# Performance work log

Hardware: AMD Instinct MI355X
Metric: run time of the kernel (lower is better)

## Reference

```python
import jax, jax.numpy as jnp
import numpy as np

N, E, IN_DIM, H, C = 100000, 1600000, 128, 4, 64
NEG_SLOPE = 0.2
BN_EPS = 1e-5


def setup_inputs() -> dict:
    key = jax.random.key(0)
    ks = jax.random.split(key, 9)
    s = 1.0 / np.sqrt(IN_DIM)
    return {
        "feature": jax.random.normal(ks[0], (N, IN_DIM), dtype=jnp.float32),
        "edge_index": jax.random.randint(ks[1], (2, E), 0, N, dtype=jnp.int64),
        "W_l": jax.random.uniform(ks[2], (IN_DIM, H * C), jnp.float32, -s, s),
        "b_l": jnp.zeros((H * C,), jnp.float32),
        "W_r": jax.random.uniform(ks[3], (IN_DIM, H * C), jnp.float32, -s, s),
        "b_r": jnp.zeros((H * C,), jnp.float32),
        "att": jax.random.normal(ks[4], (H, C), dtype=jnp.float32) * 0.1,
        "bias": jnp.zeros((H * C,), jnp.float32),
        "gamma": jnp.ones((H * C,), jnp.float32),
        "beta": jnp.zeros((H * C,), jnp.float32),
    }


def reference(feature, edge_index, W_l, b_l, W_r, b_r, att, bias, gamma, beta):
    n = feature.shape[0]
    # add self loops (add_self_loops=True)
    loops = jnp.arange(n, dtype=edge_index.dtype)
    src = jnp.concatenate([edge_index[0], loops])
    dst = jnp.concatenate([edge_index[1], loops])
    # GATv2: separate source/target linear projections -> [N, H, C]
    x_l = (feature @ W_l + b_l).reshape(n, H, C)
    x_r = (feature @ W_r + b_r).reshape(n, H, C)
    # per-edge attention score: a^T LeakyReLU(x_l[src] + x_r[dst])  [Etot, H]
    e = jax.nn.leaky_relu(x_l[src] + x_r[dst], NEG_SLOPE)
    alpha = jnp.einsum('ehc,hc->eh', e, att)
    # segment softmax over incoming edges per target node
    amax = jax.ops.segment_max(alpha, dst, num_segments=n)  # [N, H]
    alpha = jnp.exp(alpha - amax[dst])
    denom = jax.ops.segment_sum(alpha, dst, num_segments=n)  # [N, H]
    alpha = alpha / (denom[dst] + 1e-16)
    # weighted scatter-aggregate of source messages
    out = jax.ops.segment_sum(x_l[src] * alpha[:, :, None], dst, num_segments=n)
    out = out.reshape(n, H * C) + bias  # concat=True
    # BatchNorm1d (training: batch statistics over nodes)
    mean = out.mean(axis=0)
    var = out.var(axis=0)
    out = (out - mean) / jnp.sqrt(var + BN_EPS) * gamma + beta
    return jax.nn.relu(out)
```

## Files before the change

### kernel.cpp

```cpp
#include <hip/hip_runtime.h>
#include <cstdint>

#define IN_DIM 128
#define HC 256
#define NEG_SLOPE 0.2f
#define BN_EPS 1e-5f
#define LOG2E 1.44269504088896340736f

#define B_HIST 1536
#define B_CW 32
#define B_FILL 512

typedef short bf16x8 __attribute__((ext_vector_type(8)));
typedef float f32x4 __attribute__((ext_vector_type(4)));

#define EXP2F(x) __builtin_amdgcn_exp2f(x)

__device__ __forceinline__ unsigned short f2bf(float f) {
    union { float f; unsigned int u; } v; v.f = f;
    unsigned int r = (v.u + 0x7FFFu + ((v.u >> 16) & 1u)) >> 16;
    return (unsigned short)r;
}
__device__ __forceinline__ float bf2f(unsigned short h) {
    union { unsigned int u; float f; } v; v.u = ((unsigned int)h) << 16;
    return v.f;
}

template<int CTRL>
__device__ __forceinline__ float dppadd(float x) {
    int y = __builtin_amdgcn_update_dpp(0, __builtin_bit_cast(int, x), CTRL, 0xF, 0xF, true);
    return x + __builtin_bit_cast(float, y);
}
__device__ __forceinline__ float red16(float p) {
    p = dppadd<0xB1>(p);
    p = dppadd<0x4E>(p);
    p = dppadd<0x124>(p);
    p = dppadd<0x128>(p);
    return p;
}

__device__ __forceinline__ void unpk(ushort4 u, float* f) {
    f[0] = bf2f(u.x); f[1] = bf2f(u.y); f[2] = bf2f(u.z); f[3] = bf2f(u.w);
}
__device__ __forceinline__ float esc(const float* f, float x0, float x1, float x2, float x3,
                                     float4 a) {
    float z0 = f[0] + x0, z1 = f[1] + x1, z2 = f[2] + x2, z3 = f[3] + x3;
    float p = a.x * fmaxf(z0, NEG_SLOPE * z0);
    p = fmaf(a.y, fmaxf(z1, NEG_SLOPE * z1), p);
    p = fmaf(a.z, fmaxf(z2, NEG_SLOPE * z2), p);
    p = fmaf(a.w, fmaxf(z3, NEG_SLOPE * z3), p);
    return p;
}

__global__ __launch_bounds__(256) void phase1(
    const float* __restrict__ F, unsigned short* __restrict__ Afrag,
    const float* __restrict__ Wl, const float* __restrict__ Wr,
    unsigned short* __restrict__ Wfrag,
    const int* __restrict__ ei, int* __restrict__ cnt, int* __restrict__ rank,
    int E, int n, int ntiles)
{
    int b = blockIdx.x;
    if (b < B_HIST) {
        int total = E + n;
        for (int e = b * 256 + threadIdx.x; e < total; e += B_HIST * 256) {
            int dst = (e < E) ? ei[(size_t)E + e] : (e - E);
            rank[e] = atomicAdd(&cnt[dst], 1);
        }
    } else if (b < B_HIST + B_CW) {
        int ob = (b - B_HIST) * 4 + (threadIdx.x >> 6);
        int j = ob >> 2;
        int kk = ob & 3;
        int l = threadIdx.x & 63;
        int col = j * 16 + (l & 15);
        const float* W = (col < 256) ? Wl : Wr;
        int c = col & 255;
        unsigned short tmp[8];
#pragma unroll
        for (int m = 0; m < 8; ++m) {
            int k = kk * 32 + ((l >> 4) << 3) + m;
            tmp[m] = f2bf(W[(size_t)k * 256 + c]);
        }
        ulonglong2* dst = (ulonglong2*)(Wfrag + ((size_t)(j * 4 + kk) * 64 + l) * 8);
        *dst = *(ulonglong2*)tmp;
    } else {
        int i = b - B_HIST - B_CW;
        int kk = threadIdx.x >> 6;
        int l = threadIdx.x & 63;
        int row = i * 16 + (l & 15);
        int k0 = kk * 32 + ((l >> 4) << 3);
        float4 f0 = make_float4(0.f, 0.f, 0.f, 0.f), f1 = f0;
        if (row < n) {
            const float* p = F + (size_t)row * IN_DIM + k0;
            f0 = *(const float4*)p;
            f1 = *(const float4*)(p + 4);
        }
        unsigned short tmp[8];
        tmp[0] = f2bf(f0.x); tmp[1] = f2bf(f0.y); tmp[2] = f2bf(f0.z); tmp[3] = f2bf(f0.w);
        tmp[4] = f2bf(f1.x); tmp[5] = f2bf(f1.y); tmp[6] = f2bf(f1.z); tmp[7] = f2bf(f1.w);
        ulonglong2* dst = (ulonglong2*)(Afrag + ((size_t)(i * 4 + kk) * 64 + l) * 8);
        *dst = *(ulonglong2*)tmp;
    }
}

#define SCAN_BLOCKS 256

__global__ __launch_bounds__(256) void scan_phaseA(const int* __restrict__ cnt,
                                                   int* __restrict__ blocksums,
                                                   int n, int ept)
{
    __shared__ int red[256];
    int t = threadIdx.x;
    int g = blockIdx.x * 256 + t;
    int beg = g * ept, end = min(beg + ept, n);
    int s = 0;
    for (int i = beg; i < end; ++i) s += cnt[i];
    red[t] = s;
    __syncthreads();
    for (int d = 128; d > 0; d >>= 1) {
        if (t < d) red[t] += red[t + d];
        __syncthreads();
    }
    if (t == 0) blocksums[blockIdx.x] = red[0];
}

__global__ __launch_bounds__(256) void scan_phaseB(const int* __restrict__ blocksums,
                                                   int* __restrict__ blockoffs,
                                                   int* __restrict__ off, int n)
{
    __shared__ int sums[256];
    int t = threadIdx.x;
    sums[t] = blocksums[t];
    __syncthreads();
    for (int d = 1; d < 256; d <<= 1) {
        int v = (t >= d) ? sums[t - d] : 0;
        __syncthreads();
        sums[t] += v;
        __syncthreads();
    }
    blockoffs[t] = (t == 0) ? 0 : sums[t - 1];
    if (t == 255) off[n] = sums[255];
}

__global__ __launch_bounds__(256) void scan_phaseC(const int* __restrict__ cnt,
                                                   const int* __restrict__ blockoffs,
                                                   int* __restrict__ off,
                                                   int n, int ept)
{
    __shared__ int sums[256];
    int t = threadIdx.x;
    int g = blockIdx.x * 256 + t;
    int beg = g * ept, end = min(beg + ept, n);
    int s = 0;
    for (int i = beg; i < end; ++i) s += cnt[i];
    sums[t] = s;
    __syncthreads();
    for (int d = 1; d < 256; d <<= 1) {
        int v = (t >= d) ? sums[t - d] : 0;
        __syncthreads();
        sums[t] += v;
        __syncthreads();
    }
    int run = blockoffs[blockIdx.x] + ((t == 0) ? 0 : sums[t - 1]);
    for (int i = beg; i < end; ++i) {
        int c = cnt[i];
        off[i] = run;
        run += c;
    }
}

__global__ __launch_bounds__(256) void phase2(
    const unsigned short* __restrict__ Afrag, const unsigned short* __restrict__ Wfrag,
    const float* __restrict__ bl, const float* __restrict__ br,
    unsigned short* __restrict__ xl, unsigned short* __restrict__ xr,
    const int* __restrict__ ei, const int* __restrict__ rank,
    const int* __restrict__ off, int* __restrict__ csr_boff,
    int E, int n, int ntiles)
{
    int b = blockIdx.x;
    if (b < B_FILL) {
        int total = E + n;
        for (int e = b * 256 + threadIdx.x; e < total; e += B_FILL * 256) {
            int src, dst;
            if (e < E) { src = ei[e]; dst = ei[(size_t)E + e]; }
            else       { src = dst = e - E; }
            int pos = off[dst] + rank[e];
            csr_boff[pos] = src << 9;
        }
    } else {
        int i = (b - B_FILL) * 4 + (threadIdx.x >> 6);
        if (i >= ntiles) return;
        int l = threadIdx.x & 63;

        const bf16x8* av = (const bf16x8*)(Afrag + ((size_t)i * 4 * 64 + l) * 8);
        bf16x8 a0 = av[0 * 64], a1 = av[1 * 64], a2 = av[2 * 64], a3 = av[3 * 64];

        const bf16x8* wv = (const bf16x8*)Wfrag + l;
        int cl = l & 15;
        int rbase = i * 16 + ((l >> 4) << 2);

#pragma unroll 4
        for (int j = 0; j < 32; ++j) {
            const bf16x8* bp = wv + (size_t)j * 4 * 64;
            f32x4 acc = {0.f, 0.f, 0.f, 0.f};
            acc = __builtin_amdgcn_mfma_f32_16x16x32_bf16(a0, bp[0 * 64], acc, 0, 0, 0);
            acc = __builtin_amdgcn_mfma_f32_16x16x32_bf16(a1, bp[1 * 64], acc, 0, 0, 0);
            acc = __builtin_amdgcn_mfma_f32_16x16x32_bf16(a2, bp[2 * 64], acc, 0, 0, 0);
            acc = __builtin_amdgcn_mfma_f32_16x16x32_bf16(a3, bp[3 * 64], acc, 0, 0, 0);

            int col = j * 16 + cl;
            unsigned short* X = (col < 256) ? xl : xr;
            int c = col & 255;
            float bv = (col < 256) ? bl[c] : br[c];
#pragma unroll
            for (int q = 0; q < 4; ++q) {
                int row = rbase + q;
                if (row < n) X[(size_t)row * HC + c] = f2bf(acc[q] + bv);
            }
        }
    }
}

__global__ __launch_bounds__(256) void gat_agg(
    const unsigned short* __restrict__ xl, const unsigned short* __restrict__ xr,
    const int* __restrict__ csr_boff, const int* __restrict__ off,
    const float* __restrict__ att, const float* __restrict__ bias,
    float* __restrict__ out, int n)
{
    int d = (blockIdx.x * blockDim.x + threadIdx.x) >> 6;
    int lane = threadIdx.x & 63;
    if (d >= n) return;

    const char* xlc = (const char*)xl;
    int lo8 = lane << 3;
    ushort4 xru = ((const ushort4*)xr)[(size_t)d * 64 + lane];
    float xr0 = bf2f(xru.x), xr1 = bf2f(xru.y), xr2 = bf2f(xru.z), xr3 = bf2f(xru.w);
    float4 att4 = *(const float4*)(att + 4 * lane);
    att4.x *= LOG2E; att4.y *= LOG2E; att4.z *= LOG2E; att4.w *= LOG2E;

    int beg = __builtin_amdgcn_readfirstlane(off[d]);
    int end = __builtin_amdgcn_readfirstlane(off[d + 1]);
    float m = -INFINITY;
    float lsum = 0.f;
    float ax = 0.f, ay = 0.f, az = 0.f, aw = 0.f;

    int i = beg;
    for (; i + 3 < end; i += 4) {
        int b0 = __builtin_amdgcn_readfirstlane(csr_boff[i]);
        int b1 = __builtin_amdgcn_readfirstlane(csr_boff[i + 1]);
        int b2 = __builtin_amdgcn_readfirstlane(csr_boff[i + 2]);
        int b3 = __builtin_amdgcn_readfirstlane(csr_boff[i + 3]);
        ushort4 u0 = *(const ushort4*)(xlc + b0 + lo8);
        ushort4 u1 = *(const ushort4*)(xlc + b1 + lo8);
        ushort4 u2 = *(const ushort4*)(xlc + b2 + lo8);
        ushort4 u3 = *(const ushort4*)(xlc + b3 + lo8);
        float f0[4], f1[4], f2[4], f3[4];
        unpk(u0, f0); unpk(u1, f1); unpk(u2, f2); unpk(u3, f3);

        float p0 = esc(f0, xr0, xr1, xr2, xr3, att4);
        float p1 = esc(f1, xr0, xr1, xr2, xr3, att4);
        float p2 = esc(f2, xr0, xr1, xr2, xr3, att4);
        float p3 = esc(f3, xr0, xr1, xr2, xr3, att4);

        p0 = dppadd<0xB1>(p0);  p1 = dppadd<0xB1>(p1);  p2 = dppadd<0xB1>(p2);  p3 = dppadd<0xB1>(p3);
        p0 = dppadd<0x4E>(p0);  p1 = dppadd<0x4E>(p1);  p2 = dppadd<0x4E>(p2);  p3 = dppadd<0x4E>(p3);
        p0 = dppadd<0x124>(p0); p1 = dppadd<0x124>(p1); p2 = dppadd<0x124>(p2); p3 = dppadd<0x124>(p3);
        p0 = dppadd<0x128>(p0); p1 = dppadd<0x128>(p1); p2 = dppadd<0x128>(p2); p3 = dppadd<0x128>(p3);

        float mx = fmaxf(fmaxf(p0, p1), fmaxf(p2, p3));
        if (mx > m) {
            float sc = EXP2F(m - mx);
            ax *= sc; ay *= sc; az *= sc; aw *= sc; lsum *= sc;
            m = mx;
        }
        float e0 = EXP2F(p0 - m), e1 = EXP2F(p1 - m);
        float e2 = EXP2F(p2 - m), e3 = EXP2F(p3 - m);
        ax = fmaf(e0, f0[0], fmaf(e1, f1[0], fmaf(e2, f2[0], fmaf(e3, f3[0], ax))));
        ay = fmaf(e0, f0[1], fmaf(e1, f1[1], fmaf(e2, f2[1], fmaf(e3, f3[1], ay))));
        az = fmaf(e0, f0[2], fmaf(e1, f1[2], fmaf(e2, f2[2], fmaf(e3, f3[2], az))));
        aw = fmaf(e0, f0[3], fmaf(e1, f1[3], fmaf(e2, f2[3], fmaf(e3, f3[3], aw))));
        lsum += (e0 + e1) + (e2 + e3);
    }
    for (; i < end; ++i) {
        int b0 = __builtin_amdgcn_readfirstlane(csr_boff[i]);
        ushort4 u0 = *(const ushort4*)(xlc + b0 + lo8);
        float f0[4];
        unpk(u0, f0);
        float p0 = esc(f0, xr0, xr1, xr2, xr3, att4);
        p0 = red16(p0);
        if (p0 > m) {
            float sc = EXP2F(m - p0);
            ax *= sc; ay *= sc; az *= sc; aw *= sc; lsum *= sc;
            m = p0;
        }
        float e0 = EXP2F(p0 - m);
        ax = fmaf(e0, f0[0], ax); ay = fmaf(e0, f0[1], ay);
        az = fmaf(e0, f0[2], az); aw = fmaf(e0, f0[3], aw);
        lsum += e0;
    }

    float inv = 1.f / (lsum + 1e-16f);
    float4 b4 = *(const float4*)(bias + 4 * lane);
    float4 o;
    o.x = fmaf(ax, inv, b4.x); o.y = fmaf(ay, inv, b4.y);
    o.z = fmaf(az, inv, b4.z); o.w = fmaf(aw, inv, b4.w);
    *(float4*)(out + (size_t)d * HC + 4 * lane) = o;
}

#define NB_BN 1024
__global__ __launch_bounds__(256) void bn_partial(const float* __restrict__ out,
                                                  float* __restrict__ partials, int n)
{
    int c = threadIdx.x;
    int b = blockIdx.x;
    int chunk = (n + NB_BN - 1) / NB_BN;
    int beg = b * chunk;
    int end = min(beg + chunk, n);
    float s = 0.f, s2 = 0.f;
    for (int r = beg; r < end; ++r) {
        float v = out[(size_t)r * HC + c];
        s += v; s2 += v * v;
    }
    partials[(size_t)b * 512 + c] = s;
    partials[(size_t)b * 512 + 256 + c] = s2;
}

__global__ __launch_bounds__(256) void bn_final(const float* __restrict__ partials,
                                                float* __restrict__ stats, int n)
{
    int c = blockIdx.x;
    int t = threadIdx.x;
    float s = 0.f, s2 = 0.f;
    for (int b = t; b < NB_BN; b += 256) {
        s  += partials[(size_t)b * 512 + c];
        s2 += partials[(size_t)b * 512 + 256 + c];
    }
    __shared__ float rs[256], rs2[256];
    rs[t] = s; rs2[t] = s2;
    __syncthreads();
    for (int d = 128; d > 0; d >>= 1) {
        if (t < d) { rs[t] += rs[t + d]; rs2[t] += rs2[t + d]; }
        __syncthreads();
    }
    if (t == 0) {
        float mean = rs[0] / (float)n;
        float var = rs2[0] / (float)n - mean * mean;
        stats[c] = mean;
        stats[256 + c] = rsqrtf(var + BN_EPS);
    }
}

__global__ void bn_apply(float* __restrict__ out, const float* __restrict__ stats,
                         const float* __restrict__ gamma, const float* __restrict__ beta,
                         long long total4)
{
    long long stride = (long long)gridDim.x * blockDim.x;
    for (long long i = blockIdx.x * (long long)blockDim.x + threadIdx.x; i < total4;
         i += stride) {
        int cb = ((int)(i & 63)) * 4;
        float4 v = ((const float4*)out)[i];
        float4 o;
        o.x = fmaxf(0.f, (v.x - stats[cb + 0]) * stats[256 + cb + 0] * gamma[cb + 0] + beta[cb + 0]);
        o.y = fmaxf(0.f, (v.y - stats[cb + 1]) * stats[256 + cb + 1] * gamma[cb + 1] + beta[cb + 1]);
        o.z = fmaxf(0.f, (v.z - stats[cb + 2]) * stats[256 + cb + 2] * gamma[cb + 2] + beta[cb + 2]);
        o.w = fmaxf(0.f, (v.w - stats[cb + 3]) * stats[256 + cb + 3] * gamma[cb + 3] + beta[cb + 3]);
        ((float4*)out)[i] = o;
    }
}

extern "C" void kernel_launch(void* const* d_in, const int* in_sizes, int n_in,
                              void* d_out, int out_size, void* d_ws, size_t ws_size,
                              hipStream_t stream)
{
    const float* feature = (const float*)d_in[0];
    const int* ei        = (const int*)d_in[1];
    const float* Wl   = (const float*)d_in[2];
    const float* bl   = (const float*)d_in[3];
    const float* Wr   = (const float*)d_in[4];
    const float* br   = (const float*)d_in[5];
    const float* att  = (const float*)d_in[6];
    const float* bias = (const float*)d_in[7];
    const float* gamma = (const float*)d_in[8];
    const float* beta  = (const float*)d_in[9];

    const int n = in_sizes[0] / IN_DIM;
    const int E = in_sizes[1] / 2;
    const int Etot = E + n;
    const int ntiles = (n + 15) / 16;

    char* ws = (char*)d_ws;
    size_t o = 0;
    auto carve = [&](size_t bytes) -> void* {
        void* p = ws + o; o = (o + bytes + 15) & ~(size_t)15; return p;
    };
    unsigned short* xl    = (unsigned short*)carve((size_t)n * HC * sizeof(short));
    unsigned short* xr    = (unsigned short*)carve((size_t)n * HC * sizeof(short));
    unsigned short* Afrag = (unsigned short*)carve((size_t)ntiles * 4 * 64 * 8 * sizeof(short));
    unsigned short* Wfrag = (unsigned short*)carve((size_t)32 * 4 * 64 * 8 * sizeof(short));
    int*   csr_boff = (int*)carve((size_t)Etot * sizeof(int));
    int*   rank    = (int*)carve((size_t)Etot * sizeof(int));
    int*   cnt     = (int*)carve((size_t)n * sizeof(int));
    int*   off     = (int*)carve((size_t)(n + 1) * sizeof(int));
    int*   blocksums = (int*)carve(SCAN_BLOCKS * sizeof(int));
    int*   blockoffs = (int*)carve(SCAN_BLOCKS * sizeof(int));
    float* partials = (float*)carve((size_t)NB_BN * 512 * sizeof(float));
    float* stats   = (float*)carve(512 * sizeof(float));
    float* outf = (float*)d_out;

    if (o > ws_size) return;

    (void)hipMemsetAsync(cnt, 0, (size_t)n * sizeof(int), stream);

    phase1<<<B_HIST + B_CW + ntiles, 256, 0, stream>>>(
        feature, Afrag, Wl, Wr, Wfrag, ei, cnt, rank, E, n, ntiles);

    int ept = (n + SCAN_BLOCKS * 256 - 1) / (SCAN_BLOCKS * 256);
    scan_phaseA<<<SCAN_BLOCKS, 256, 0, stream>>>(cnt, blocksums, n, ept);
    scan_phaseB<<<1, 256, 0, stream>>>(blocksums, blockoffs, off, n);
    scan_phaseC<<<SCAN_BLOCKS, 256, 0, stream>>>(cnt, blockoffs, off, n, ept);

    phase2<<<B_FILL + (ntiles + 3) / 4, 256, 0, stream>>>(
        Afrag, Wfrag, bl, br, xl, xr, ei, rank, off, csr_boff, E, n, ntiles);

    int agg_blocks = (n + 3) / 4;
    gat_agg<<<agg_blocks, 256, 0, stream>>>(xl, xr, csr_boff, off, att, bias, outf, n);

    bn_partial<<<NB_BN, 256, 0, stream>>>(outf, partials, n);
    bn_final<<<256, 256, 0, stream>>>(partials, stats, n);
    long long total4 = (long long)n * (HC / 4);
    bn_apply<<<4096, 256, 0, stream>>>(outf, stats, gamma, beta, total4);
}
```

Measured before the change: 391.6 us.

## Store aggregation output as bf16, prefetch gathers, fold scan phase B

The aggregation kernel now writes its pre-BatchNorm output as bf16 into a workspace buffer. The BN partial and apply kernels read that bf16 buffer, and apply writes the final fp32 output, which halves intermediate traffic. The gather loop in gat_agg is software-pipelined so the next four neighbour rows load while the current ones are computed. The single-block scan phase B is merged into phase C, with every block redundantly scanning the block sums, which removes one launch. The bf16 intermediate lowers precision before the BN statistics are computed.

```diff
diff --git a/kernel.cpp b/kernel.cpp
--- a/kernel.cpp
+++ b/kernel.cpp
@@ -123,31 +123,15 @@
     if (t == 0) blocksums[blockIdx.x] = red[0];
 }
 
-__global__ __launch_bounds__(256) void scan_phaseB(const int* __restrict__ blocksums,
-                                                   int* __restrict__ blockoffs,
-                                                   int* __restrict__ off, int n)
-{
+__global__ __launch_bounds__(256) void scan_phaseC(const int* __restrict__ cnt,
+                                                   const int* __restrict__ blocksums,
+                                                   int* __restrict__ off,
+                                                   int n, int ept)
+{
+    __shared__ int bs[256];
     __shared__ int sums[256];
     int t = threadIdx.x;
-    sums[t] = blocksums[t];
-    __syncthreads();
-    for (int d = 1; d < 256; d <<= 1) {
-        int v = (t >= d) ? sums[t - d] : 0;
-        __syncthreads();
-        sums[t] += v;
-        __syncthreads();
-    }
-    blockoffs[t] = (t == 0) ? 0 : sums[t - 1];
-    if (t == 255) off[n] = sums[255];
-}
-
-__global__ __launch_bounds__(256) void scan_phaseC(const int* __restrict__ cnt,
-                                                   const int* __restrict__ blockoffs,
-                                                   int* __restrict__ off,
-                                                   int n, int ept)
-{
-    __shared__ int sums[256];
-    int t = threadIdx.x;
+    bs[t] = blocksums[t];
     int g = blockIdx.x * 256 + t;
     int beg = g * ept, end = min(beg + ept, n);
     int s = 0;
@@ -155,17 +139,21 @@
     sums[t] = s;
     __syncthreads();
     for (int d = 1; d < 256; d <<= 1) {
-        int v = (t >= d) ? sums[t - d] : 0;
+        int v1 = (t >= d) ? sums[t - d] : 0;
+        int v2 = (t >= d) ? bs[t - d] : 0;
         __syncthreads();
-        sums[t] += v;
+        sums[t] += v1;
+        bs[t] += v2;
         __syncthreads();
     }
-    int run = blockoffs[blockIdx.x] + ((t == 0) ? 0 : sums[t - 1]);
+    int blockoff = (blockIdx.x == 0) ? 0 : bs[blockIdx.x - 1];
+    int run = blockoff + ((t == 0) ? 0 : sums[t - 1]);
     for (int i = beg; i < end; ++i) {
         int c = cnt[i];
         off[i] = run;
         run += c;
     }
+    if (blockIdx.x == 0 && t == 0) off[n] = bs[255];
 }
 
 __global__ __launch_bounds__(256) void phase2(
@@ -224,7 +212,7 @@
     const unsigned short* __restrict__ xl, const unsigned short* __restrict__ xr,
     const int* __restrict__ csr_boff, const int* __restrict__ off,
     const float* __restrict__ att, const float* __restrict__ bias,
-    float* __restrict__ out, int n)
+    unsigned short* __restrict__ outb, int n)
 {
     int d = (blockIdx.x * blockDim.x + threadIdx.x) >> 6;
     int lane = threadIdx.x & 63;
@@ -243,18 +231,36 @@
     float lsum = 0.f;
     float ax = 0.f, ay = 0.f, az = 0.f, aw = 0.f;
 
+    int nmain = (end - beg) & ~3;
+    int imend = beg + nmain;
     int i = beg;
-    for (; i + 3 < end; i += 4) {
+
+    ushort4 u0, u1, u2, u3;
+    if (i < imend) {
         int b0 = __builtin_amdgcn_readfirstlane(csr_boff[i]);
         int b1 = __builtin_amdgcn_readfirstlane(csr_boff[i + 1]);
         int b2 = __builtin_amdgcn_readfirstlane(csr_boff[i + 2]);
         int b3 = __builtin_amdgcn_readfirstlane(csr_boff[i + 3]);
-        ushort4 u0 = *(const ushort4*)(xlc + b0 + lo8);
-        ushort4 u1 = *(const ushort4*)(xlc + b1 + lo8);
-        ushort4 u2 = *(const ushort4*)(xlc + b2 + lo8);
-        ushort4 u3 = *(const ushort4*)(xlc + b3 + lo8);
+        u0 = *(const ushort4*)(xlc + b0 + lo8);
+        u1 = *(const ushort4*)(xlc + b1 + lo8);
+        u2 = *(const ushort4*)(xlc + b2 + lo8);
+        u3 = *(const ushort4*)(xlc + b3 + lo8);
+    }
+    while (i < imend) {
+        ushort4 c0 = u0, c1 = u1, c2 = u2, c3 = u3;
+        int inext = i + 4;
+        if (inext < imend) {
+            int b0 = __builtin_amdgcn_readfirstlane(csr_boff[inext]);
+            int b1 = __builtin_amdgcn_readfirstlane(csr_boff[inext + 1]);
+            int b2 = __builtin_amdgcn_readfirstlane(csr_boff[inext + 2]);
+            int b3 = __builtin_amdgcn_readfirstlane(csr_boff[inext + 3]);
+            u0 = *(const ushort4*)(xlc + b0 + lo8);
+            u1 = *(const ushort4*)(xlc + b1 + lo8);
+            u2 = *(const ushort4*)(xlc + b2 + lo8);
+            u3 = *(const ushort4*)(xlc + b3 + lo8);
+        }
         float f0[4], f1[4], f2[4], f3[4];
-        unpk(u0, f0); unpk(u1, f1); unpk(u2, f2); unpk(u3, f3);
+        unpk(c0, f0); unpk(c1, f1); unpk(c2, f2); unpk(c3, f3);
 
         float p0 = esc(f0, xr0, xr1, xr2, xr3, att4);
         float p1 = esc(f1, xr0, xr1, xr2, xr3, att4);
@@ -279,12 +285,13 @@
         az = fmaf(e0, f0[2], fmaf(e1, f1[2], fmaf(e2, f2[2], fmaf(e3, f3[2], az))));
         aw = fmaf(e0, f0[3], fmaf(e1, f1[3], fmaf(e2, f2[3], fmaf(e3, f3[3], aw))));
         lsum += (e0 + e1) + (e2 + e3);
+        i = inext;
     }
     for (; i < end; ++i) {
         int b0 = __builtin_amdgcn_readfirstlane(csr_boff[i]);
-        ushort4 u0 = *(const ushort4*)(xlc + b0 + lo8);
+        ushort4 t0 = *(const ushort4*)(xlc + b0 + lo8);
         float f0[4];
-        unpk(u0, f0);
+        unpk(t0, f0);
         float p0 = esc(f0, xr0, xr1, xr2, xr3, att4);
         p0 = red16(p0);
         if (p0 > m) {
@@ -300,14 +307,16 @@
 
     float inv = 1.f / (lsum + 1e-16f);
     float4 b4 = *(const float4*)(bias + 4 * lane);
-    float4 o;
-    o.x = fmaf(ax, inv, b4.x); o.y = fmaf(ay, inv, b4.y);
-    o.z = fmaf(az, inv, b4.z); o.w = fmaf(aw, inv, b4.w);
-    *(float4*)(out + (size_t)d * HC + 4 * lane) = o;
+    ushort4 o;
+    o.x = f2bf(fmaf(ax, inv, b4.x));
+    o.y = f2bf(fmaf(ay, inv, b4.y));
+    o.z = f2bf(fmaf(az, inv, b4.z));
+    o.w = f2bf(fmaf(aw, inv, b4.w));
+    ((ushort4*)outb)[(size_t)d * 64 + lane] = o;
 }
 
 #define NB_BN 1024
-__global__ __launch_bounds__(256) void bn_partial(const float* __restrict__ out,
+__global__ __launch_bounds__(256) void bn_partial(const unsigned short* __restrict__ outb,
                                                   float* __restrict__ partials, int n)
 {
     int c = threadIdx.x;
@@ -317,7 +326,7 @@
     int end = min(beg + chunk, n);
     float s = 0.f, s2 = 0.f;
     for (int r = beg; r < end; ++r) {
-        float v = out[(size_t)r * HC + c];
+        float v = bf2f(outb[(size_t)r * HC + c]);
         s += v; s2 += v * v;
     }
     partials[(size_t)b * 512 + c] = s;
@@ -349,20 +358,21 @@
     }
 }
 
-__global__ void bn_apply(float* __restrict__ out, const float* __restrict__ stats,
+__global__ void bn_apply(const unsigned short* __restrict__ outb,
+                         const float* __restrict__ stats,
                          const float* __restrict__ gamma, const float* __restrict__ beta,
-                         long long total4)
+                         float* __restrict__ out, long long total4)
 {
     long long stride = (long long)gridDim.x * blockDim.x;
     for (long long i = blockIdx.x * (long long)blockDim.x + threadIdx.x; i < total4;
          i += stride) {
         int cb = ((int)(i & 63)) * 4;
-        float4 v = ((const float4*)out)[i];
+        ushort4 u = ((const ushort4*)outb)[i];
         float4 o;
-        o.x = fmaxf(0.f, (v.x - stats[cb + 0]) * stats[256 + cb + 0] * gamma[cb + 0] + beta[cb + 0]);
-        o.y = fmaxf(0.f, (v.y - stats[cb + 1]) * stats[256 + cb + 1] * gamma[cb + 1] + beta[cb + 1]);
-        o.z = fmaxf(0.f, (v.z - stats[cb + 2]) * stats[256 + cb + 2] * gamma[cb + 2] + beta[cb + 2]);
-        o.w = fmaxf(0.f, (v.w - stats[cb + 3]) * stats[256 + cb + 3] * gamma[cb + 3] + beta[cb + 3]);
+        o.x = fmaxf(0.f, (bf2f(u.x) - stats[cb + 0]) * stats[256 + cb + 0] * gamma[cb + 0] + beta[cb + 0]);
+        o.y = fmaxf(0.f, (bf2f(u.y) - stats[cb + 1]) * stats[256 + cb + 1] * gamma[cb + 1] + beta[cb + 1]);
+        o.z = fmaxf(0.f, (bf2f(u.z) - stats[cb + 2]) * stats[256 + cb + 2] * gamma[cb + 2] + beta[cb + 2]);
+        o.w = fmaxf(0.f, (bf2f(u.w) - stats[cb + 3]) * stats[256 + cb + 3] * gamma[cb + 3] + beta[cb + 3]);
         ((float4*)out)[i] = o;
     }
 }
@@ -394,6 +404,7 @@
     };
     unsigned short* xl    = (unsigned short*)carve((size_t)n * HC * sizeof(short));
     unsigned short* xr    = (unsigned short*)carve((size_t)n * HC * sizeof(short));
+    unsigned short* outb  = (unsigned short*)carve((size_t)n * HC * sizeof(short));
     unsigned short* Afrag = (unsigned short*)carve((size_t)ntiles * 4 * 64 * 8 * sizeof(short));
     unsigned short* Wfrag = (unsigned short*)carve((size_t)32 * 4 * 64 * 8 * sizeof(short));
     int*   csr_boff = (int*)carve((size_t)Etot * sizeof(int));
@@ -401,7 +412,6 @@
     int*   cnt     = (int*)carve((size_t)n * sizeof(int));
     int*   off     = (int*)carve((size_t)(n + 1) * sizeof(int));
     int*   blocksums = (int*)carve(SCAN_BLOCKS * sizeof(int));
-    int*   blockoffs = (int*)carve(SCAN_BLOCKS * sizeof(int));
     float* partials = (float*)carve((size_t)NB_BN * 512 * sizeof(float));
     float* stats   = (float*)carve(512 * sizeof(float));
     float* outf = (float*)d_out;
@@ -415,17 +425,16 @@
 
     int ept = (n + SCAN_BLOCKS * 256 - 1) / (SCAN_BLOCKS * 256);
     scan_phaseA<<<SCAN_BLOCKS, 256, 0, stream>>>(cnt, blocksums, n, ept);
-    scan_phaseB<<<1, 256, 0, stream>>>(blocksums, blockoffs, off, n);
-    scan_phaseC<<<SCAN_BLOCKS, 256, 0, stream>>>(cnt, blockoffs, off, n, ept);
+    scan_phaseC<<<SCAN_BLOCKS, 256, 0, stream>>>(cnt, blocksums, off, n, ept);
 
     phase2<<<B_FILL + (ntiles + 3) / 4, 256, 0, stream>>>(
         Afrag, Wfrag, bl, br, xl, xr, ei, rank, off, csr_boff, E, n, ntiles);
 
     int agg_blocks = (n + 3) / 4;
-    gat_agg<<<agg_blocks, 256, 0, stream>>>(xl, xr, csr_boff, off, att, bias, outf, n);
-
-    bn_partial<<<NB_BN, 256, 0, stream>>>(outf, partials, n);
+    gat_agg<<<agg_blocks, 256, 0, stream>>>(xl, xr, csr_boff, off, att, bias, outb, n);
+
+    bn_partial<<<NB_BN, 256, 0, stream>>>(outb, partials, n);
     bn_final<<<256, 256, 0, stream>>>(partials, stats, n);
     long long total4 = (long long)n * (HC / 4);
-    bn_apply<<<4096, 256, 0, stream>>>(outf, stats, gamma, beta, total4);
-}
+    bn_apply<<<4096, 256, 0, stream>>>(outb, stats, gamma, beta, outf, total4);
+}
```

Result: faster. 374.5 us (-4.4%).
